# Kernel optimization log

Measured on AMD Instinct MI355X. Metric: run time of the kernel, lower is better.

## Reference

```python
import jax, jax.numpy as jnp
import numpy as np

KEY_DIM, VALUE_DIM, NUM_HEAD, OUT_DIM = 128, 64, 4, 64
HEAD_KDIM = KEY_DIM // NUM_HEAD   # 32
HEAD_VDIM = VALUE_DIM // NUM_HEAD # 16

def _xavier(key, shape):
    # xavier_uniform over (fan_in=shape[0], fan_out=prod(shape[1:])) like torch
    fan_in, fan_out = shape[0], int(np.prod(shape[1:]))
    lim = float(np.sqrt(6.0 / (fan_in + fan_out)))
    return jax.random.uniform(key, shape, jnp.float32, -lim, lim)

def setup_inputs() -> dict:
    key = jax.random.key(0)
    ks = jax.random.split(key, 7)
    B, Q, K = 2, 4096, 4096
    return {
        "q_data": jax.random.normal(ks[0], (B, Q, KEY_DIM), jnp.float32),
        "m_data": jax.random.normal(ks[1], (B, K, VALUE_DIM), jnp.float32),
        "mask": jax.random.randint(ks[2], (B, K), 0, 2, jnp.int32),
        "q_weights": _xavier(ks[3], (KEY_DIM, NUM_HEAD, HEAD_KDIM)),
        "k_weights": _xavier(ks[4], (VALUE_DIM, NUM_HEAD, HEAD_KDIM)),
        "v_weights": _xavier(ks[5], (VALUE_DIM, NUM_HEAD, HEAD_VDIM)),
        "o_weights": _xavier(ks[6], (NUM_HEAD, HEAD_VDIM, OUT_DIM)),
        "o_bias": jnp.zeros((OUT_DIM,), jnp.float32),
    }

def reference(q_data, m_data, mask, q_weights, k_weights, v_weights, o_weights, o_bias):
    head_kdim = q_weights.shape[-1]
    scale = head_kdim ** (-0.5)
    Q = jnp.einsum('bqa,ahc->bqhc', q_data, q_weights) * scale
    K = jnp.einsum('bka,ahc->bkhc', m_data, k_weights)
    V = jnp.einsum('bka,ahc->bkhc', m_data, v_weights)
    logits = jnp.einsum('bqhc,bkhc->bhqk', Q, K)
    neg = jnp.finfo(logits.dtype).min
    logits = jnp.where(mask[:, None, None, :] == 0, neg, logits)
    weights = jax.nn.softmax(logits, axis=-1)
    weight_avg = jnp.einsum('bhqk,bkhc->bqhc', weights, V)
    return jnp.einsum('bqhc,hco->bqo', weight_avg, o_weights) + o_bias
```

## Files before the change

kernel.cpp:

```cpp
#include <hip/hip_runtime.h>
#include <stdint.h>

#define B_  2
#define QN  4096
#define KN  4096
#define AD  128
#define MD  64
#define H_  4
#define C_  32
#define CV  16
#define OD  64

typedef short bf16x8 __attribute__((ext_vector_type(8)));
typedef short bf16x4 __attribute__((ext_vector_type(4)));
typedef float f32x4  __attribute__((ext_vector_type(4)));

__device__ __forceinline__ short f2bf(float f) {
  union { float f; unsigned u; } v; v.f = f;
  unsigned r = v.u + 0x7fffu + ((v.u >> 16) & 1u);
  return (short)(r >> 16);
}
__device__ __forceinline__ unsigned pack2t(float a, float b) {
  union { float f; unsigned u; } ua, ub; ua.f = a; ub.f = b;
  return __builtin_amdgcn_perm(ub.u, ua.u, 0x07060302u);
}
__device__ __forceinline__ bf16x4 pack4t(f32x4 p) {
  union { unsigned u[2]; bf16x4 v; } t;
  t.u[0] = pack2t(p[0], p[1]); t.u[1] = pack2t(p[2], p[3]);
  return t.v;
}
__device__ __forceinline__ bf16x8 cvt8(f32x4 a, f32x4 b) {
  bf16x8 o;
  o[0]=f2bf(a[0]); o[1]=f2bf(a[1]); o[2]=f2bf(a[2]); o[3]=f2bf(a[3]);
  o[4]=f2bf(b[0]); o[5]=f2bf(b[1]); o[6]=f2bf(b[2]); o[7]=f2bf(b[3]);
  return o;
}

__global__ __launch_bounds__(256) void k_proj(const float* __restrict__ qdf, const float* __restrict__ mdf,
                                              const float* __restrict__ qwf, const float* __restrict__ kwf,
                                              const float* __restrict__ vwf,
                                              const int* __restrict__ mask, int* __restrict__ kc,
                                              short* __restrict__ Qp, short* __restrict__ Kp,
                                              short* __restrict__ Vpt) {
  const int lane = threadIdx.x & 63;
  const int wid = threadIdx.x >> 6;
  const int n = lane & 15, quad = lane >> 4;
  const f32x4 z4 = {0.f,0.f,0.f,0.f};
  if (blockIdx.x < 1024) {
    const int t = blockIdx.x*4 + wid;
    const int rt = t >> 3, ct = t & 7;
    const int row = rt*16 + n;
    const int hc0 = ct*16;
    f32x4 acc = z4;
    #pragma unroll
    for (int ak = 0; ak < 4; ++ak) {
      const int a0 = ak*32 + quad*8;
      const float* ap = qdf + row*AD + a0;
      bf16x8 afrag = cvt8(*(const f32x4*)ap, *(const f32x4*)(ap + 4));
      bf16x8 bfrag;
      #pragma unroll
      for (int j = 0; j < 8; ++j) bfrag[j] = f2bf(qwf[(a0 + j)*128 + hc0 + n]);
      acc = __builtin_amdgcn_mfma_f32_16x16x32_bf16(afrag, bfrag, acc, 0, 0, 0);
    }
    const int h = hc0 >> 5, c0 = (hc0 & 31) + n;
    const float s = 0.17677669529663687f * 1.44269504088896341f;
    #pragma unroll
    for (int r = 0; r < 4; ++r) {
      const int rr = rt*16 + quad*4 + r;
      const int bb = rr >> 12, q = rr & 4095;
      Qp[((bb*H_ + h)*QN + q)*C_ + c0] = f2bf(acc[r] * s);
    }
    return;
  }
  __shared__ unsigned long long balS[64];
  __shared__ int pref[64];
  __shared__ int kcS;
  const int bidx = blockIdx.x - 1024;
  const int b = (bidx*4) / 3072;
  #pragma unroll
  for (int p = 0; p < 16; ++p) {
    const int seg = wid*16 + p;
    const unsigned long long bal = __ballot(mask[b*KN + seg*64 + lane] != 0);
    if (lane == 0) balS[seg] = bal;
  }
  __syncthreads();
  if (wid == 0) {
    int v = __popcll(balS[lane]); int incl = v;
    for (int d = 1; d < 64; d <<= 1) { int o = __shfl_up(incl, d); if (lane >= d) incl += o; }
    pref[lane] = incl - v;
    if (lane == 63) kcS = incl;
  }
  __syncthreads();
  const int Kc = kcS;
  const int nch = (Kc + 31) >> 5;
  const int t = bidx*4 + wid;
  const int rem = t - b*3072;
  const int rt = rem / 12, ct = rem - rt*12;
  if (rem == 0 && lane == 0) kc[b] = Kc;
  if (rt*16 >= nch*32) return;
  const int j = rt*16 + n;
  const int valid = (j < Kc);
  int src = 0;
  if (valid) {
    int seg = 0;
    #pragma unroll
    for (int st = 32; st >= 1; st >>= 1)
      if (seg + st < 64 && pref[seg + st] <= j) seg += st;
    int r2 = j - pref[seg];
    unsigned long long m = balS[seg];
    int pos = 0;
    #pragma unroll
    for (int w = 32; w >= 1; w >>= 1) {
      const int c = __popcll(m & ((1ull << w) - 1ull));
      if (r2 >= c) { r2 -= c; m >>= w; pos += w; }
    }
    src = seg*64 + pos;
  }
  const float* mrow = mdf + (b*KN + src)*MD;
  const int hc = ct*16 + n;
  f32x4 acc = z4;
  #pragma unroll
  for (int ch = 0; ch < 2; ++ch) {
    const int a0 = ch*32 + quad*8;
    bf16x8 afrag = cvt8(*(const f32x4*)(mrow + a0), *(const f32x4*)(mrow + a0 + 4));
    if (!valid) {
      #pragma unroll
      for (int jj = 0; jj < 8; ++jj) afrag[jj] = 0;
    }
    bf16x8 bfrag;
    if (ct < 8) {
      #pragma unroll
      for (int jj = 0; jj < 8; ++jj) bfrag[jj] = f2bf(kwf[(a0 + jj)*128 + hc]);
    } else {
      #pragma unroll
      for (int jj = 0; jj < 8; ++jj) bfrag[jj] = f2bf(vwf[(a0 + jj)*64 + hc - 128]);
    }
    acc = __builtin_amdgcn_mfma_f32_16x16x32_bf16(afrag, bfrag, acc, 0, 0, 0);
  }
  if (ct < 8) {
    const int h = hc >> 5, c = hc & 31;
    #pragma unroll
    for (int r = 0; r < 4; ++r) {
      const int jj2 = rt*16 + quad*4 + r;
      Kp[((b*H_ + h)*KN + jj2)*C_ + c] = f2bf(acc[r]);
    }
  } else {
    const int hc2 = hc - 128; const int h = hc2 >> 4, cv = hc2 & 15;
    bf16x4 pk; pk[0]=f2bf(acc[0]); pk[1]=f2bf(acc[1]); pk[2]=f2bf(acc[2]); pk[3]=f2bf(acc[3]);
    *(bf16x4*)(Vpt + ((b*H_ + h)*CV + cv)*KN + rt*16 + quad*4) = pk;
  }
}

__global__ __launch_bounds__(1024) void k_attn(const short* __restrict__ Qp, const short* __restrict__ Kp,
                                               const short* __restrict__ Vpt, const int* __restrict__ kc,
                                               const float* __restrict__ w2f, const float* __restrict__ obf,
                                               float* __restrict__ out) {
  __shared__ __attribute__((aligned(16))) char pool[40960];
  const int lane = threadIdx.x & 63, wid = threadIdx.x >> 6;
  const int h = wid & 3, split = wid >> 2;
  const int flatq = blockIdx.x * 32;
  const int b = flatq >> 12, qt = flatq & 4095;
  const int bh = b*H_ + h;
  const int n = lane & 15, quad = lane >> 4;
  const short* Qb = Qp + (bh*QN + qt)*C_;
  const short* Kb = Kp + bh*KN*C_;
  const short* Vb = Vpt + bh*CV*KN;
  const bf16x8 qb0 = *(const bf16x8*)(Qb + n*C_ + quad*8);
  const bf16x8 qb1 = *(const bf16x8*)(Qb + (16 + n)*C_ + quad*8);
  const int Kc = kc[b];
  const int nch = (Kc + 31) >> 5;
  const f32x4 z4 = {0.f,0.f,0.f,0.f};
  f32x4 o0 = z4, o1 = z4;
  float l0 = 0.f, l1 = 0.f;
  short* Pw = (short*)(pool + wid*2560);

  auto loadK = [&](int cc, bf16x8& f0, bf16x8& f1, bf16x8& v) {
    const int kb = cc*32;
    f0 = *(const bf16x8*)(Kb + (kb + n)*C_ + quad*8);
    f1 = *(const bf16x8*)(Kb + (kb + 16 + n)*C_ + quad*8);
    v  = *(const bf16x8*)(Vb + n*KN + kb + quad*8);
  };
  auto consume = [&](const bf16x8& ckf0, const bf16x8& ckf1, const bf16x8& cva) {
    f32x4 s00 = __builtin_amdgcn_mfma_f32_16x16x32_bf16(ckf0, qb0, z4, 0, 0, 0);
    f32x4 s01 = __builtin_amdgcn_mfma_f32_16x16x32_bf16(ckf0, qb1, z4, 0, 0, 0);
    f32x4 s10 = __builtin_amdgcn_mfma_f32_16x16x32_bf16(ckf1, qb0, z4, 0, 0, 0);
    f32x4 s11 = __builtin_amdgcn_mfma_f32_16x16x32_bf16(ckf1, qb1, z4, 0, 0, 0);
    f32x4 p00, p01, p10, p11;
    #pragma unroll
    for (int r = 0; r < 4; ++r) {
      p00[r] = __builtin_amdgcn_exp2f(s00[r]);
      p01[r] = __builtin_amdgcn_exp2f(s01[r]);
      p10[r] = __builtin_amdgcn_exp2f(s10[r]);
      p11[r] = __builtin_amdgcn_exp2f(s11[r]);
    }
    l0 += ((p00[0]+p00[1])+(p00[2]+p00[3])) + ((p10[0]+p10[1])+(p10[2]+p10[3]));
    l1 += ((p01[0]+p01[1])+(p01[2]+p01[3])) + ((p11[0]+p11[1])+(p11[2]+p11[3]));
    *(bf16x4*)(Pw + n*40 + quad*4)           = pack4t(p00);
    *(bf16x4*)(Pw + n*40 + 16 + quad*4)      = pack4t(p10);
    *(bf16x4*)(Pw + (16+n)*40 + quad*4)      = pack4t(p01);
    *(bf16x4*)(Pw + (16+n)*40 + 16 + quad*4) = pack4t(p11);
    const bf16x8 pb0 = *(const bf16x8*)(Pw + n*40 + quad*8);
    const bf16x8 pb1 = *(const bf16x8*)(Pw + (16+n)*40 + quad*8);
    o0 = __builtin_amdgcn_mfma_f32_16x16x32_bf16(cva, pb0, o0, 0, 0, 0);
    o1 = __builtin_amdgcn_mfma_f32_16x16x32_bf16(cva, pb1, o1, 0, 0, 0);
  };

  bf16x8 k00, k01, v0, k10, k11, v1, k20, k21, v2;
  int ci = split;
  if (ci < nch)     loadK(ci,     k00, k01, v0);
  if (ci + 4 < nch) loadK(ci + 4, k10, k11, v1);
  for (; ci < nch; ci += 12) {
    if (ci + 8 < nch) loadK(ci + 8, k20, k21, v2);
    consume(k00, k01, v0);
    if (ci + 4 < nch) {
      if (ci + 12 < nch) loadK(ci + 12, k00, k01, v0);
      consume(k10, k11, v1);
      if (ci + 8 < nch) {
        if (ci + 16 < nch) loadK(ci + 16, k10, k11, v1);
        consume(k20, k21, v2);
      }
    }
  }
  __syncthreads();
  float* Of   = (float*)pool;
  float* Lb   = (float*)(pool + 33280);
  short* ObfA = (short*)(pool + 35328);
  #pragma unroll
  for (int r = 0; r < 4; ++r) {
    const int hc = h*16 + quad*4 + r;
    Of[split*2080 + n*65 + hc]      = o0[r];
    Of[split*2080 + (16+n)*65 + hc] = o1[r];
  }
  l0 += __shfl_xor(l0, 16); l0 += __shfl_xor(l0, 32);
  l1 += __shfl_xor(l1, 16); l1 += __shfl_xor(l1, 32);
  if (lane < 16) {
    Lb[split*128 + h*32 + lane]      = l0;
    Lb[split*128 + h*32 + 16 + lane] = l1;
  }
  __syncthreads();
  {
    const float npad = (float)(nch*32 - Kc);
    const int e = threadIdx.x * 2;
    const int q = e >> 6, hc = e & 63;
    const int hh = hc >> 4;
    const float l = (Lb[hh*32 + q] + Lb[128 + hh*32 + q])
                  + (Lb[256 + hh*32 + q] + Lb[384 + hh*32 + q]) - npad;
    const float inv = 1.00135f / l;
    const float v0_ = ((Of[q*65 + hc]     + Of[2080 + q*65 + hc])
                     + (Of[4160 + q*65 + hc] + Of[6240 + q*65 + hc])) * inv;
    const float v1_ = ((Of[q*65 + hc + 1] + Of[2080 + q*65 + hc + 1])
                     + (Of[4160 + q*65 + hc + 1] + Of[6240 + q*65 + hc + 1])) * inv;
    union { unsigned u; short s[2]; } pk;
    pk.s[0] = f2bf(v0_); pk.s[1] = f2bf(v1_);
    *(unsigned*)(ObfA + q*72 + hc) = pk.u;
  }
  __syncthreads();
  if (wid < 8) {
    const int mt = wid & 1, nt = wid >> 1;
    f32x4 acc = z4;
    #pragma unroll
    for (int kchunk = 0; kchunk < 2; ++kchunk) {
      const bf16x8 afrag = *(const bf16x8*)(ObfA + (mt*16 + n)*72 + kchunk*32 + quad*8);
      bf16x8 bfrag;
      #pragma unroll
      for (int jj = 0; jj < 8; ++jj)
        bfrag[jj] = f2bf(w2f[(kchunk*32 + quad*8 + jj)*64 + nt*16 + n]);
      acc = __builtin_amdgcn_mfma_f32_16x16x32_bf16(afrag, bfrag, acc, 0, 0, 0);
    }
    const int ocol = nt*16 + n;
    const float bias = obf[ocol];
    #pragma unroll
    for (int r = 0; r < 4; ++r) {
      const int qg = flatq + mt*16 + quad*4 + r;
      out[qg*64 + ocol] = acc[r] + bias;
    }
  }
}

extern "C" void kernel_launch(void* const* d_in, const int* in_sizes, int n_in,
                              void* d_out, int out_size, void* d_ws, size_t ws_size,
                              hipStream_t stream) {
  const float* qd  = (const float*)d_in[0];
  const float* md  = (const float*)d_in[1];
  const int*   msk = (const int*)  d_in[2];
  const float* qw  = (const float*)d_in[3];
  const float* kw  = (const float*)d_in[4];
  const float* vw  = (const float*)d_in[5];
  const float* ow  = (const float*)d_in[6];
  const float* ob  = (const float*)d_in[7];
  float* out = (float*)d_out;

  char* ws = (char*)d_ws;
  int*   kc  = (int*)  (ws);
  short* Qp  = (short*)(ws + (64<<10));
  short* Kp  = (short*)(ws + (64<<10) + (2u<<20));
  short* Vpt = (short*)(ws + (64<<10) + (4u<<20));

  hipLaunchKernelGGL(k_proj, dim3(2560), dim3(256),  0, stream, qd, md, qw, kw, vw, msk, kc, Qp, Kp, Vpt);
  hipLaunchKernelGGL(k_attn, dim3(256),  dim3(1024), 0, stream, Qp, Kp, Vpt, kc, ow, ob, out);
}
```

Measured before the change: 102.6 us.

## Fuse Q projection into attention kernel via shared memory

Moves the Q projection out of the projection kernel and into the attention kernel. Each attention block computes its 32 query rows times 128 head channels with MFMA, stores them scaled to bf16 in shared memory, and reads per-head fragments from there. This removes the global write and re-read of Qp and shrinks the first kernel's grid. In exchange the attention kernel gains a prologue, extra shared memory and a block barrier, and its critical path gets longer.

```diff
diff --git a/kernel.cpp b/kernel.cpp
--- a/kernel.cpp
+++ b/kernel.cpp
@@ -36,47 +36,20 @@
   return o;
 }
 
-__global__ __launch_bounds__(256) void k_proj(const float* __restrict__ qdf, const float* __restrict__ mdf,
-                                              const float* __restrict__ qwf, const float* __restrict__ kwf,
+__global__ __launch_bounds__(256) void k_proj(const float* __restrict__ mdf,
+                                              const float* __restrict__ kwf,
                                               const float* __restrict__ vwf,
                                               const int* __restrict__ mask, int* __restrict__ kc,
-                                              short* __restrict__ Qp, short* __restrict__ Kp,
-                                              short* __restrict__ Vpt) {
+                                              short* __restrict__ Kp, short* __restrict__ Vpt) {
+  __shared__ unsigned long long balS[64];
+  __shared__ int pref[64];
+  __shared__ int kcS;
   const int lane = threadIdx.x & 63;
   const int wid = threadIdx.x >> 6;
   const int n = lane & 15, quad = lane >> 4;
   const f32x4 z4 = {0.f,0.f,0.f,0.f};
-  if (blockIdx.x < 1024) {
-    const int t = blockIdx.x*4 + wid;
-    const int rt = t >> 3, ct = t & 7;
-    const int row = rt*16 + n;
-    const int hc0 = ct*16;
-    f32x4 acc = z4;
-    #pragma unroll
-    for (int ak = 0; ak < 4; ++ak) {
-      const int a0 = ak*32 + quad*8;
-      const float* ap = qdf + row*AD + a0;
-      bf16x8 afrag = cvt8(*(const f32x4*)ap, *(const f32x4*)(ap + 4));
-      bf16x8 bfrag;
-      #pragma unroll
-      for (int j = 0; j < 8; ++j) bfrag[j] = f2bf(qwf[(a0 + j)*128 + hc0 + n]);
-      acc = __builtin_amdgcn_mfma_f32_16x16x32_bf16(afrag, bfrag, acc, 0, 0, 0);
-    }
-    const int h = hc0 >> 5, c0 = (hc0 & 31) + n;
-    const float s = 0.17677669529663687f * 1.44269504088896341f;
-    #pragma unroll
-    for (int r = 0; r < 4; ++r) {
-      const int rr = rt*16 + quad*4 + r;
-      const int bb = rr >> 12, q = rr & 4095;
-      Qp[((bb*H_ + h)*QN + q)*C_ + c0] = f2bf(acc[r] * s);
-    }
-    return;
-  }
-  __shared__ unsigned long long balS[64];
-  __shared__ int pref[64];
-  __shared__ int kcS;
-  const int bidx = blockIdx.x - 1024;
-  const int b = (bidx*4) / 3072;
+  const int bidx = blockIdx.x;
+  const int b = bidx / 768;
   #pragma unroll
   for (int p = 0; p < 16; ++p) {
     const int seg = wid*16 + p;
@@ -151,25 +124,49 @@
   }
 }
 
-__global__ __launch_bounds__(1024) void k_attn(const short* __restrict__ Qp, const short* __restrict__ Kp,
-                                               const short* __restrict__ Vpt, const int* __restrict__ kc,
-                                               const float* __restrict__ w2f, const float* __restrict__ obf,
+__global__ __launch_bounds__(1024) void k_attn(const float* __restrict__ qdf,
+                                               const float* __restrict__ qwf,
+                                               const short* __restrict__ Kp,
+                                               const short* __restrict__ Vpt,
+                                               const int* __restrict__ kc,
+                                               const float* __restrict__ w2f,
+                                               const float* __restrict__ obf,
                                                float* __restrict__ out) {
   __shared__ __attribute__((aligned(16))) char pool[40960];
+  __shared__ __attribute__((aligned(16))) short QL[32*136];
   const int lane = threadIdx.x & 63, wid = threadIdx.x >> 6;
   const int h = wid & 3, split = wid >> 2;
   const int flatq = blockIdx.x * 32;
-  const int b = flatq >> 12, qt = flatq & 4095;
+  const int b = flatq >> 12;
   const int bh = b*H_ + h;
   const int n = lane & 15, quad = lane >> 4;
-  const short* Qb = Qp + (bh*QN + qt)*C_;
-  const short* Kb = Kp + bh*KN*C_;
-  const short* Vb = Vpt + bh*CV*KN;
-  const bf16x8 qb0 = *(const bf16x8*)(Qb + n*C_ + quad*8);
-  const bf16x8 qb1 = *(const bf16x8*)(Qb + (16 + n)*C_ + quad*8);
   const int Kc = kc[b];
   const int nch = (Kc + 31) >> 5;
   const f32x4 z4 = {0.f,0.f,0.f,0.f};
+  {
+    const int mt = wid & 1, ct = wid >> 1;
+    const int row = flatq + mt*16 + n;
+    f32x4 acc = z4;
+    #pragma unroll
+    for (int ak = 0; ak < 4; ++ak) {
+      const int a0 = ak*32 + quad*8;
+      const float* ap = qdf + row*AD + a0;
+      bf16x8 afrag = cvt8(*(const f32x4*)ap, *(const f32x4*)(ap + 4));
+      bf16x8 bfrag;
+      #pragma unroll
+      for (int j = 0; j < 8; ++j) bfrag[j] = f2bf(qwf[(a0 + j)*128 + ct*16 + n]);
+      acc = __builtin_amdgcn_mfma_f32_16x16x32_bf16(afrag, bfrag, acc, 0, 0, 0);
+    }
+    const float s = 0.17677669529663687f * 1.44269504088896341f;
+    #pragma unroll
+    for (int r = 0; r < 4; ++r)
+      QL[(mt*16 + quad*4 + r)*136 + ct*16 + n] = f2bf(acc[r] * s);
+  }
+  __syncthreads();
+  const bf16x8 qb0 = *(const bf16x8*)(QL + n*136 + h*32 + quad*8);
+  const bf16x8 qb1 = *(const bf16x8*)(QL + (16 + n)*136 + h*32 + quad*8);
+  const short* Kb = Kp + bh*KN*C_;
+  const short* Vb = Vpt + bh*CV*KN;
   f32x4 o0 = z4, o1 = z4;
   float l0 = 0.f, l1 = 0.f;
   short* Pw = (short*)(pool + wid*2560);
@@ -292,10 +289,9 @@
 
   char* ws = (char*)d_ws;
   int*   kc  = (int*)  (ws);
-  short* Qp  = (short*)(ws + (64<<10));
-  short* Kp  = (short*)(ws + (64<<10) + (2u<<20));
-  short* Vpt = (short*)(ws + (64<<10) + (4u<<20));
-
-  hipLaunchKernelGGL(k_proj, dim3(2560), dim3(256),  0, stream, qd, md, qw, kw, vw, msk, kc, Qp, Kp, Vpt);
-  hipLaunchKernelGGL(k_attn, dim3(256),  dim3(1024), 0, stream, Qp, Kp, Vpt, kc, ow, ob, out);
-}
+  short* Kp  = (short*)(ws + (64<<10));
+  short* Vpt = (short*)(ws + (64<<10) + (2u<<20));
+
+  hipLaunchKernelGGL(k_proj, dim3(1536), dim3(256),  0, stream, md, kw, vw, msk, kc, Kp, Vpt);
+  hipLaunchKernelGGL(k_attn, dim3(256),  dim3(1024), 0, stream, qd, qw, Kp, Vpt, kc, ow, ob, out);
+}
```

After: 102.1 us. Within noise of the previous version (-0.5%).
